# Optimization experiments

Measured on AMD Instinct MI355X. Metric: run time of the kernel, lower is better.

## Reference

```python
import jax, jax.numpy as jnp
import numpy as np

HEADS = 12
DIM_HEAD = 64
SCALE = DIM_HEAD ** -0.5


def _layer_norm(x, w):
    # LayerNorm with learned weight and zero bias (bias is a frozen zeros buffer)
    mu = jnp.mean(x, axis=-1, keepdims=True)
    var = jnp.var(x, axis=-1, keepdims=True)
    return (x - mu) * jax.lax.rsqrt(var + 1e-5) * w


def setup_inputs() -> dict:
    key = jax.random.key(0)
    ks = jax.random.split(key, 6)
    b, n, j, dim = 4, 2048, 2048, 768
    inner = HEADS * DIM_HEAD  # 768
    return {
        "x": jax.random.normal(ks[0], (b, n, dim), dtype=jnp.float32),
        "context": jax.random.normal(ks[1], (b, j, dim), dtype=jnp.float32),
        "mask": jnp.zeros((b, n, j), dtype=jnp.float32),
        "ln_w": jnp.ones((dim,), dtype=jnp.float32),
        "Wq": jax.random.normal(ks[2], (dim, inner), dtype=jnp.float32) * (dim ** -0.5),
        "Wkv": jax.random.normal(ks[3], (dim, 2 * DIM_HEAD), dtype=jnp.float32) * (dim ** -0.5),
        "Wo": jax.random.normal(ks[4], (inner, dim), dtype=jnp.float32) * (inner ** -0.5),
    }


def reference(x, context, mask, ln_w, Wq, Wkv, Wo):
    b, n, dim = x.shape
    xn = _layer_norm(x, ln_w)
    # context_norm is Identity (norm_context=False)
    q = xn @ Wq  # [b, n, h*d]
    q = q.reshape(b, n, HEADS, DIM_HEAD).transpose(0, 2, 1, 3) * SCALE  # [b,h,n,d]
    kv = context @ Wkv  # [b, j, 2d]
    k, v = jnp.split(kv, 2, axis=-1)  # each [b, j, d] (multi-query: shared K/V)
    sim = jnp.einsum('bhid,bjd->bhij', q, k) + mask[:, None, :, :]
    # softmax with max-subtraction (jax.nn.softmax is max-stabilized, same math)
    attn = jax.nn.softmax(sim, axis=-1)
    out = jnp.einsum('bhij,bjd->bhid', attn, v)
    out = out.transpose(0, 2, 1, 3).reshape(b, n, HEADS * DIM_HEAD)
    out = out @ Wo
    # ff is None (parallel_ff=False)
    return out
```

## Files before the change

kernel.cpp:

```cpp
#include <hip/hip_runtime.h>


typedef unsigned short u16;
typedef unsigned int u32;
typedef __attribute__((ext_vector_type(8))) short short8;
typedef __attribute__((ext_vector_type(4))) short short4v;
typedef __attribute__((ext_vector_type(4))) float f32x4;
typedef __attribute__((ext_vector_type(2))) u32 u32x2;

#define L2E 1.44269504088896340736f

__device__ __forceinline__ u16 f2bf(float f) {
  u32 u = __float_as_uint(f);
  u += 0x7FFFu + ((u >> 16) & 1u);
  return (u16)(u >> 16);
}
__device__ __forceinline__ f32x4 mfma16(short8 a, short8 b, f32x4 c) {
  return __builtin_amdgcn_mfma_f32_16x16x32_bf16(a, b, c, 0, 0, 0);
}
__device__ __forceinline__ f32x4 mfma16k16(short4v a, short4v b, f32x4 c) {
  return __builtin_amdgcn_mfma_f32_16x16x16bf16_1k(a, b, c, 0, 0, 0);
}
__device__ __forceinline__ void gl2lds16(const u16* g, u16* s) {
  __builtin_amdgcn_global_load_lds(
      (const __attribute__((address_space(1))) u32*)g,
      (__attribute__((address_space(3))) u32*)s, 16, 0, 0);
}
__device__ __forceinline__ u32 pk2bf(float a, float b) {
  return ((__float_as_uint(a) + 0x8000u) >> 16) |
         ((__float_as_uint(b) + 0x8000u) & 0xffff0000u);
}

__device__ __forceinline__ void wt_tile(const float* in, u16* out, int K,
                                        int N, int tn, int tk,
                                        u16 (*tile)[72]) {
  const int t = threadIdx.x;
  const int tn0 = tn * 64, tk0 = tk * 64;
#pragma unroll
  for (int p = 0; p < 16; p++) {
    int e = p * 256 + t;
    int k = e >> 6, n = e & 63;
    tile[n][k] = f2bf(in[(size_t)(tk0 + k) * N + tn0 + n]);
  }
  __syncthreads();
#pragma unroll
  for (int p = 0; p < 16; p++) {
    int e = p * 256 + t;
    int n = e >> 6, k = e & 63;
    out[(size_t)(tn0 + n) * K + tk0 + k] = tile[n][k];
  }
}

__global__ __launch_bounds__(256)
void prep_kernel(const float* __restrict__ Wq, const float* __restrict__ Wkv,
                 const float* __restrict__ Wo, const float* __restrict__ ctx,
                 const float* __restrict__ x, const float* __restrict__ lnw,
                 u16* __restrict__ WqT, u16* __restrict__ WkvT,
                 u16* __restrict__ WoT, u16* __restrict__ ctxb,
                 u16* __restrict__ xn) {
  __shared__ u16 tile[64][72];
  __shared__ float red[8];
  __shared__ float sh_mu, sh_rs;
  const int bid = blockIdx.x, t = threadIdx.x;
  if (bid < 288) {
    const float* in = bid < 144 ? Wq : Wo;
    u16* out = bid < 144 ? WqT : WoT;
    int id = bid < 144 ? bid : bid - 144;
    wt_tile(in, out, 768, 768, id % 12, id / 12, tile);
  } else if (bid < 312) {
    int id = bid - 288;
    wt_tile(Wkv, WkvT, 768, 128, id % 2, id / 2, tile);
  } else if (bid < 6456) {
    int i = (bid - 312) * 256 + t;
    float4 v = ((const float4*)ctx)[i];
    ushort4 o;
    o.x = f2bf(v.x); o.y = f2bf(v.y); o.z = f2bf(v.z); o.w = f2bf(v.w);
    ((ushort4*)ctxb)[i] = o;
  } else {
    const int row = bid - 6456;
    const float* xr = x + (size_t)row * 768;
    float v0 = xr[t], v1 = xr[t + 256], v2 = xr[t + 512];
    float s = v0 + v1 + v2;
    float q = v0 * v0 + v1 * v1 + v2 * v2;
#pragma unroll
    for (int off = 32; off; off >>= 1) {
      s += __shfl_down(s, off);
      q += __shfl_down(q, off);
    }
    int wv = t >> 6;
    if ((t & 63) == 0) { red[wv * 2] = s; red[wv * 2 + 1] = q; }
    __syncthreads();
    if (t == 0) {
      float S = red[0] + red[2] + red[4] + red[6];
      float Q = red[1] + red[3] + red[5] + red[7];
      float mu = S * (1.0f / 768.0f);
      float var = Q * (1.0f / 768.0f) - mu * mu;
      sh_mu = mu;
      sh_rs = rsqrtf(var + 1e-5f);
    }
    __syncthreads();
    float mu = sh_mu, rs = sh_rs;
    u16* o = xn + (size_t)row * 768;
    o[t]       = f2bf((v0 - mu) * rs * lnw[t]);
    o[t + 256] = f2bf((v1 - mu) * rs * lnw[t + 256]);
    o[t + 512] = f2bf((v2 - mu) * rs * lnw[t + 512]);
  }
}

template <int BM, int BN>
__device__ __forceinline__ void gemm_stage(const u16* A, const u16* Bt, int K,
                                           int m0, int n0, int k0, u16* As,
                                           u16* Bs, int w, int l) {
  constexpr int CHA = BM * 8;
  constexpr int ISS = (BM + BN) * 8 / 256;
#pragma unroll
  for (int i = 0; i < ISS; i++) {
    const int c0 = (i * 4 + w) * 64;
    const int c = c0 + l;
    if (c0 < CHA) {
      int row = c >> 3, cc = c & 7, gc = cc ^ (row & 7);
      gl2lds16(A + (size_t)(m0 + row) * K + k0 + gc * 8, As + c0 * 8);
    } else {
      int cb = c - CHA;
      int row = cb >> 3, cc = cb & 7, gc = cc ^ (row & 7);
      gl2lds16(Bt + (size_t)(n0 + row) * K + k0 + gc * 8, Bs + (c0 - CHA) * 8);
    }
  }
}

template <int BM, int BN>
__device__ __forceinline__ void gemm_core(u16* As0, u16* As1, u16* Bs0,
                                          u16* Bs1, const u16* A,
                                          const u16* Bt, void* C, int N, int K,
                                          float scale, int out_bf16, int bx,
                                          int by) {
  constexpr int MT = BM / 32, NT = BN / 32;
  const int t = threadIdx.x;
  const int w = t >> 6, l = t & 63, lg = l >> 4, lc = l & 15;
  const int wm = w & 1, wn = w >> 1;
  const int n0 = bx * BN, m0 = by * BM;
  u16* Asb[2] = {As0, As1};
  u16* Bsb[2] = {Bs0, Bs1};

  f32x4 acc[MT][NT];
#pragma unroll
  for (int mt = 0; mt < MT; mt++)
#pragma unroll
    for (int nt = 0; nt < NT; nt++) acc[mt][nt] = (f32x4){0.f, 0.f, 0.f, 0.f};

  gemm_stage<BM, BN>(A, Bt, K, m0, n0, 0, As0, Bs0, w, l);
  int p = 0;
  for (int k0 = 0; k0 < K; k0 += 64, p ^= 1) {
    __syncthreads();
    if (k0 + 64 < K)
      gemm_stage<BM, BN>(A, Bt, K, m0, n0, k0 + 64, Asb[p ^ 1], Bsb[p ^ 1], w, l);
    const u16* As = Asb[p];
    const u16* Bs = Bsb[p];
#pragma unroll
    for (int ks = 0; ks < 2; ks++) {
      short8 af[MT], bfr[NT];
#pragma unroll
      for (int mt = 0; mt < MT; mt++) {
        int m = wm * (BM / 2) + mt * 16 + lc;
        af[mt] = *(const short8*)&As[m * 64 + (((ks * 4 + lg) ^ (m & 7)) * 8)];
      }
#pragma unroll
      for (int nt = 0; nt < NT; nt++) {
        int n = wn * (BN / 2) + nt * 16 + lc;
        bfr[nt] = *(const short8*)&Bs[n * 64 + (((ks * 4 + lg) ^ (n & 7)) * 8)];
      }
#pragma unroll
      for (int mt = 0; mt < MT; mt++)
#pragma unroll
        for (int nt = 0; nt < NT; nt++)
          acc[mt][nt] = mfma16(af[mt], bfr[nt], acc[mt][nt]);
    }
  }

#pragma unroll
  for (int mt = 0; mt < MT; mt++)
#pragma unroll
    for (int nt = 0; nt < NT; nt++)
#pragma unroll
      for (int r = 0; r < 4; r++) {
        int row = m0 + wm * (BM / 2) + mt * 16 + lg * 4 + r;
        int col = n0 + wn * (BN / 2) + nt * 16 + lc;
        float v = acc[mt][nt][r] * scale;
        if (out_bf16)
          ((u16*)C)[(size_t)row * N + col] = f2bf(v);
        else
          ((float*)C)[(size_t)row * N + col] = v;
      }
}

__global__ __launch_bounds__(256)
void gemm_qkv_kernel(const u16* __restrict__ xn, const u16* __restrict__ WqT,
                     u16* __restrict__ qb, const u16* __restrict__ ctxb,
                     const u16* __restrict__ WkvT, u16* __restrict__ kvb) {
  __shared__ __align__(16) u16 As[2][128 * 64];
  __shared__ __align__(16) u16 Bs[2][64 * 64];
  if (blockIdx.x < 12)
    gemm_core<128, 64>(As[0], As[1], Bs[0], Bs[1], xn, WqT, qb, 768, 768,
                       0.125f * L2E, 1, blockIdx.x, blockIdx.y);
  else
    gemm_core<128, 64>(As[0], As[1], Bs[0], Bs[1], ctxb, WkvT, kvb, 128, 768,
                       1.0f, 1, blockIdx.x - 12, blockIdx.y);
}

__global__ __launch_bounds__(256)
void gemm_o_kernel(const u16* __restrict__ aob, const u16* __restrict__ WoT,
                   float* __restrict__ out) {
  __shared__ __align__(16) u16 As[2][128 * 64];
  __shared__ __align__(16) u16 Bs[2][64 * 64];
  gemm_core<128, 64>(As[0], As[1], Bs[0], Bs[1], aob, WoT, out, 768, 768, 1.0f,
                     0, blockIdx.x, blockIdx.y);
}

__global__ void tv_kernel(const u16* __restrict__ kv, u16* __restrict__ vT) {
  __shared__ u16 tile[64][72];
  const int t = threadIdx.x;
  const int bb = blockIdx.y, j0 = blockIdx.x << 6;
#pragma unroll
  for (int p = 0; p < 16; p++) {
    int e = p * 256 + t;
    int j = e >> 6, d = e & 63;
    tile[j][d] = kv[(size_t)(bb * 2048 + j0 + j) * 128 + 64 + d];
  }
  __syncthreads();
#pragma unroll
  for (int p = 0; p < 16; p++) {
    int e = p * 256 + t;
    int d = e >> 6, j = e & 63;
    vT[(size_t)(bb * 64 + d) * 2048 + j0 + j] = tile[j][d];
  }
}

__device__ __forceinline__ void attn_stage(const u16* kvb, const u16* vtb,
                                           u16* Kq, u16* Vq, int j0, int w,
                                           int l) {
#pragma unroll
  for (int i = 0; i < 2; i++) {
    int c = i * 64 + l;
    int row = c >> 3, cc = c & 7, gc = cc ^ (row & 7);
    gl2lds16(kvb + (size_t)(j0 + w * 16 + row) * 128 + gc * 8,
             Kq + i * 64 * 8);
  }
#pragma unroll
  for (int i = 0; i < 2; i++) {
    int c = i * 64 + l;
    int d = c >> 1, hf = c & 1;
    gl2lds16(vtb + (size_t)d * 2048 + j0 + w * 16 + hf * 8, Vq + i * 64 * 8);
  }
}

__global__ __launch_bounds__(256, 3)
void attn_kernel(const u16* __restrict__ q, const u16* __restrict__ kv,
                 const u16* __restrict__ vT, const float* __restrict__ mask,
                 u16* __restrict__ ao) {
  __shared__ __align__(16) u16 lds[2][4][2048];

  const int t = threadIdx.x;
  const int i0 = blockIdx.x << 4;
  const int bb = blockIdx.y;
  const int hg = blockIdx.z;
  const int w = t >> 6, l = t & 63, lg = l >> 4, lc = l & 15;

  short8 qf[4][2];
#pragma unroll
  for (int hh = 0; hh < 4; hh++) {
    const int h = hg * 4 + hh;
    const u16* qp = q + (size_t)(bb * 2048 + i0 + lc) * 768 + h * 64 + lg * 8;
    qf[hh][0] = *(const short8*)qp;
    qf[hh][1] = *(const short8*)(qp + 32);
  }

  f32x4 o[4][4];
  float lsum[4] = {0.f, 0.f, 0.f, 0.f};
#pragma unroll
  for (int hh = 0; hh < 4; hh++)
#pragma unroll
    for (int nt = 0; nt < 4; nt++) o[hh][nt] = (f32x4){0.f, 0.f, 0.f, 0.f};

  const u16* kvb = kv + (size_t)bb * 2048 * 128;
  const u16* vtb = vT + (size_t)bb * 64 * 2048;
  const float* mrow =
      mask + (size_t)(bb * 2048 + i0 + lc) * 2048 + w * 16 + lg * 4;

  attn_stage(kvb, vtb, &lds[0][w][0], &lds[0][w][1024], 0, w, l);
  float4 mk = *(const float4*)mrow;

  for (int jj = 0; jj < 32; jj++) {
    const int p = jj & 1;
    __syncthreads();
    float4 mk_n = mk;
    if (jj + 1 < 32) {
      attn_stage(kvb, vtb, &lds[p ^ 1][w][0], &lds[p ^ 1][w][1024],
                 (jj + 1) * 64, w, l);
      mk_n = *(const float4*)(mrow + (jj + 1) * 64);
    }
    const u16* Kq = &lds[p][w][0];
    const u16* Vq = &lds[p][w][1024];
    short8 kf0 = *(const short8*)&Kq[lc * 64 + ((lg ^ (lc & 7)) * 8)];
    short8 kf1 = *(const short8*)&Kq[lc * 64 + (((4 + lg) ^ (lc & 7)) * 8)];
    short4v vfr[4];
#pragma unroll
    for (int nt = 0; nt < 4; nt++)
      vfr[nt] = *(const short4v*)&Vq[(nt * 16 + lc) * 16 + lg * 4];

#pragma unroll
    for (int hh = 0; hh < 4; hh++) {
      f32x4 s = mfma16(kf0, qf[hh][0], (f32x4){0.f, 0.f, 0.f, 0.f});
      s = mfma16(kf1, qf[hh][1], s);
      float p0 = __builtin_amdgcn_exp2f(__builtin_fmaf(mk.x, L2E, s[0]));
      float p1 = __builtin_amdgcn_exp2f(__builtin_fmaf(mk.y, L2E, s[1]));
      float p2 = __builtin_amdgcn_exp2f(__builtin_fmaf(mk.z, L2E, s[2]));
      float p3 = __builtin_amdgcn_exp2f(__builtin_fmaf(mk.w, L2E, s[3]));
      lsum[hh] += (p0 + p1) + (p2 + p3);
      u32x2 pp = {pk2bf(p0, p1), pk2bf(p2, p3)};
      short4v pk = __builtin_bit_cast(short4v, pp);
#pragma unroll
      for (int nt = 0; nt < 4; nt++)
        o[hh][nt] = mfma16k16(pk, vfr[nt], o[hh][nt]);
    }
    mk = mk_n;
  }

  float* f = (float*)&lds[0][0][0];
  const int ei = t >> 4, eg = t & 15;
#pragma unroll
  for (int hh = 0; hh < 4; hh++) {
    float lt = lsum[hh];
    lt += __shfl_xor(lt, 16);
    lt += __shfl_xor(lt, 32);
    __syncthreads();
    if (lg == 0) f[4096 + w * 16 + lc] = lt;
#pragma unroll
    for (int nt = 0; nt < 4; nt++)
#pragma unroll
      for (int r = 0; r < 4; r++)
        f[w * 1024 + (lg * 4 + r) * 64 + nt * 16 + lc] = o[hh][nt][r];
    __syncthreads();
    f32x4 sum = *(const f32x4*)&f[ei * 64 + eg * 4];
#pragma unroll
    for (int ww = 1; ww < 4; ww++) {
      f32x4 v2 = *(const f32x4*)&f[ww * 1024 + ei * 64 + eg * 4];
      sum[0] += v2[0]; sum[1] += v2[1]; sum[2] += v2[2]; sum[3] += v2[3];
    }
    float ltot = f[4096 + ei] + f[4096 + 16 + ei] + f[4096 + 32 + ei] +
                 f[4096 + 48 + ei];
    float inv = 1.0f / ltot;
    ushort4 ov;
    ov.x = f2bf(sum[0] * inv);
    ov.y = f2bf(sum[1] * inv);
    ov.z = f2bf(sum[2] * inv);
    ov.w = f2bf(sum[3] * inv);
    const int h = hg * 4 + hh;
    *(ushort4*)&ao[(size_t)(bb * 2048 + i0 + ei) * 768 + h * 64 + eg * 4] = ov;
  }
}

extern "C" void kernel_launch(void* const* d_in, const int* in_sizes, int n_in,
                              void* d_out, int out_size, void* d_ws,
                              size_t ws_size, hipStream_t stream) {
  const float* x    = (const float*)d_in[0];
  const float* ctx  = (const float*)d_in[1];
  const float* mask = (const float*)d_in[2];
  const float* lnw  = (const float*)d_in[3];
  const float* Wq   = (const float*)d_in[4];
  const float* Wkv  = (const float*)d_in[5];
  const float* Wo   = (const float*)d_in[6];

  char* ws = (char*)d_ws;
  u16* WqT  = (u16*)(ws + 0);
  u16* WkvT = (u16*)(ws + 1179648);
  u16* WoT  = (u16*)(ws + 1376256);
  u16* xn   = (u16*)(ws + 2555904);
  u16* ctxb = (u16*)(ws + 15138816);
  u16* qb   = (u16*)(ws + 27721728);
  u16* kvb  = (u16*)(ws + 40304640);
  u16* vTb  = (u16*)(ws + 42401792);
  u16* aob  = (u16*)(ws + 43450368);

  hipLaunchKernelGGL(prep_kernel, dim3(14648), dim3(256), 0, stream,
                     Wq, Wkv, Wo, ctx, x, lnw, WqT, WkvT, WoT, ctxb, xn);
  hipLaunchKernelGGL(gemm_qkv_kernel, dim3(14, 64), dim3(256), 0, stream,
                     xn, WqT, qb, ctxb, WkvT, kvb);
  hipLaunchKernelGGL(tv_kernel, dim3(32, 4), dim3(256), 0, stream, kvb, vTb);
  hipLaunchKernelGGL(attn_kernel, dim3(128, 4, 3), dim3(256), 0, stream,
                     qb, kvb, vTb, mask, aob);
  hipLaunchKernelGGL(gemm_o_kernel, dim3(12, 64), dim3(256), 0, stream,
                     aob, WoT, (float*)d_out);
}
```

Baseline: 291.4 us.

## Prepack K/V into MFMA fragment layout and load directly to registers

Replaces the V-transpose kernel with a pack kernel that writes K and V in per-lane MFMA fragment order. The attention kernel then drops the LDS staging and per-iteration barriers, loading fragments straight from global memory into registers with a one-step register prefetch. It also swaps the manual bf16 packing for the hardware v_cvt_pk_bf16_f32 instruction. The cost is exposed global-load latency, with only one iteration of prefetch and no shared staging, and the packed buffers reuse the ctxb region of the workspace.

```diff
diff --git a/kernel.cpp b/kernel.cpp
--- a/kernel.cpp
+++ b/kernel.cpp
@@ -26,9 +26,12 @@
       (const __attribute__((address_space(1))) u32*)g,
       (__attribute__((address_space(3))) u32*)s, 16, 0, 0);
 }
-__device__ __forceinline__ u32 pk2bf(float a, float b) {
-  return ((__float_as_uint(a) + 0x8000u) >> 16) |
-         ((__float_as_uint(b) + 0x8000u) & 0xffff0000u);
+__device__ __forceinline__ short4v cvt4bf(float a, float b, float c, float d) {
+  u32 lo, hi;
+  asm("v_cvt_pk_bf16_f32 %0, %1, %2" : "=v"(lo) : "v"(a), "v"(b));
+  asm("v_cvt_pk_bf16_f32 %0, %1, %2" : "=v"(hi) : "v"(c), "v"(d));
+  u32x2 pp = {lo, hi};
+  return __builtin_bit_cast(short4v, pp);
 }
 
 __device__ __forceinline__ void wt_tile(const float* in, u16* out, int K,
@@ -216,48 +219,39 @@
                      0, blockIdx.x, blockIdx.y);
 }
 
-__global__ void tv_kernel(const u16* __restrict__ kv, u16* __restrict__ vT) {
-  __shared__ u16 tile[64][72];
-  const int t = threadIdx.x;
-  const int bb = blockIdx.y, j0 = blockIdx.x << 6;
-#pragma unroll
-  for (int p = 0; p < 16; p++) {
-    int e = p * 256 + t;
-    int j = e >> 6, d = e & 63;
-    tile[j][d] = kv[(size_t)(bb * 2048 + j0 + j) * 128 + 64 + d];
-  }
-  __syncthreads();
-#pragma unroll
-  for (int p = 0; p < 16; p++) {
-    int e = p * 256 + t;
-    int d = e >> 6, j = e & 63;
-    vT[(size_t)(bb * 64 + d) * 2048 + j0 + j] = tile[j][d];
-  }
-}
-
-__device__ __forceinline__ void attn_stage(const u16* kvb, const u16* vtb,
-                                           u16* Kq, u16* Vq, int j0, int w,
-                                           int l) {
-#pragma unroll
-  for (int i = 0; i < 2; i++) {
-    int c = i * 64 + l;
-    int row = c >> 3, cc = c & 7, gc = cc ^ (row & 7);
-    gl2lds16(kvb + (size_t)(j0 + w * 16 + row) * 128 + gc * 8,
-             Kq + i * 64 * 8);
-  }
-#pragma unroll
-  for (int i = 0; i < 2; i++) {
-    int c = i * 64 + l;
-    int d = c >> 1, hf = c & 1;
-    gl2lds16(vtb + (size_t)d * 2048 + j0 + w * 16 + hf * 8, Vq + i * 64 * 8);
+__global__ void pack_kernel(const u16* __restrict__ kv, u16* __restrict__ kF,
+                            u16* __restrict__ vF) {
+  const int t = threadIdx.x, l = t & 63, cw = t >> 6;
+  const int b = blockIdx.y, jb0 = blockIdx.x * 4;
+  const int lc = l & 15, lg = l >> 4;
+#pragma unroll
+  for (int c = cw; c < 8; c += 4) {
+    int jb = jb0 + (c >> 1), half = c & 1;
+    const u16* src =
+        kv + (size_t)(b * 2048 + jb * 16 + lc) * 128 + half * 32 + lg * 8;
+    u16* dst = kF + (((size_t)(b * 128 + jb) * 2 + half) * 64 + l) * 8;
+    *(short8*)dst = *(const short8*)src;
+  }
+#pragma unroll
+  for (int c = cw; c < 8; c += 4) {
+    int jb = jb0 + (c >> 1), ntp = c & 1;
+    u16 tmp[8];
+#pragma unroll
+    for (int e = 0; e < 8; e++) {
+      int d = ntp * 32 + (e >> 2) * 16 + lc;
+      int j = jb * 16 + lg * 4 + (e & 3);
+      tmp[e] = kv[(size_t)(b * 2048 + j) * 128 + 64 + d];
+    }
+    u16* dst = vF + (((size_t)(b * 128 + jb) * 2 + ntp) * 64 + l) * 8;
+    *(short8*)dst = *(const short8*)tmp;
   }
 }
 
 __global__ __launch_bounds__(256, 3)
-void attn_kernel(const u16* __restrict__ q, const u16* __restrict__ kv,
-                 const u16* __restrict__ vT, const float* __restrict__ mask,
+void attn_kernel(const u16* __restrict__ q, const u16* __restrict__ kF,
+                 const u16* __restrict__ vF, const float* __restrict__ mask,
                  u16* __restrict__ ao) {
-  __shared__ __align__(16) u16 lds[2][4][2048];
+  __shared__ float f[4160];
 
   const int t = threadIdx.x;
   const int i0 = blockIdx.x << 4;
@@ -281,51 +275,48 @@
 #pragma unroll
     for (int nt = 0; nt < 4; nt++) o[hh][nt] = (f32x4){0.f, 0.f, 0.f, 0.f};
 
-  const u16* kvb = kv + (size_t)bb * 2048 * 128;
-  const u16* vtb = vT + (size_t)bb * 64 * 2048;
+  const u16* kb = kF + ((size_t)(bb * 128 + w) * 2) * 512 + l * 8;
+  const u16* vb = vF + ((size_t)(bb * 128 + w) * 2) * 512 + l * 8;
   const float* mrow =
       mask + (size_t)(bb * 2048 + i0 + lc) * 2048 + w * 16 + lg * 4;
 
-  attn_stage(kvb, vtb, &lds[0][w][0], &lds[0][w][1024], 0, w, l);
+  short8 kc0 = *(const short8*)(kb);
+  short8 kc1 = *(const short8*)(kb + 512);
+  short8 vc0 = *(const short8*)(vb);
+  short8 vc1 = *(const short8*)(vb + 512);
   float4 mk = *(const float4*)mrow;
 
   for (int jj = 0; jj < 32; jj++) {
-    const int p = jj & 1;
-    __syncthreads();
-    float4 mk_n = mk;
-    if (jj + 1 < 32) {
-      attn_stage(kvb, vtb, &lds[p ^ 1][w][0], &lds[p ^ 1][w][1024],
-                 (jj + 1) * 64, w, l);
-      mk_n = *(const float4*)(mrow + (jj + 1) * 64);
-    }
-    const u16* Kq = &lds[p][w][0];
-    const u16* Vq = &lds[p][w][1024];
-    short8 kf0 = *(const short8*)&Kq[lc * 64 + ((lg ^ (lc & 7)) * 8)];
-    short8 kf1 = *(const short8*)&Kq[lc * 64 + (((4 + lg) ^ (lc & 7)) * 8)];
+    const int jn = jj < 31 ? jj + 1 : 31;
+    short8 kn0 = *(const short8*)(kb + (size_t)jn * 4096);
+    short8 kn1 = *(const short8*)(kb + (size_t)jn * 4096 + 512);
+    short8 vn0 = *(const short8*)(vb + (size_t)jn * 4096);
+    short8 vn1 = *(const short8*)(vb + (size_t)jn * 4096 + 512);
+    float4 mkn = *(const float4*)(mrow + (size_t)jn * 64);
+
     short4v vfr[4];
-#pragma unroll
-    for (int nt = 0; nt < 4; nt++)
-      vfr[nt] = *(const short4v*)&Vq[(nt * 16 + lc) * 16 + lg * 4];
+    vfr[0] = __builtin_shufflevector(vc0, vc0, 0, 1, 2, 3);
+    vfr[1] = __builtin_shufflevector(vc0, vc0, 4, 5, 6, 7);
+    vfr[2] = __builtin_shufflevector(vc1, vc1, 0, 1, 2, 3);
+    vfr[3] = __builtin_shufflevector(vc1, vc1, 4, 5, 6, 7);
 
 #pragma unroll
     for (int hh = 0; hh < 4; hh++) {
-      f32x4 s = mfma16(kf0, qf[hh][0], (f32x4){0.f, 0.f, 0.f, 0.f});
-      s = mfma16(kf1, qf[hh][1], s);
+      f32x4 s = mfma16(kc0, qf[hh][0], (f32x4){0.f, 0.f, 0.f, 0.f});
+      s = mfma16(kc1, qf[hh][1], s);
       float p0 = __builtin_amdgcn_exp2f(__builtin_fmaf(mk.x, L2E, s[0]));
       float p1 = __builtin_amdgcn_exp2f(__builtin_fmaf(mk.y, L2E, s[1]));
       float p2 = __builtin_amdgcn_exp2f(__builtin_fmaf(mk.z, L2E, s[2]));
       float p3 = __builtin_amdgcn_exp2f(__builtin_fmaf(mk.w, L2E, s[3]));
       lsum[hh] += (p0 + p1) + (p2 + p3);
-      u32x2 pp = {pk2bf(p0, p1), pk2bf(p2, p3)};
-      short4v pk = __builtin_bit_cast(short4v, pp);
+      short4v pk = cvt4bf(p0, p1, p2, p3);
 #pragma unroll
       for (int nt = 0; nt < 4; nt++)
         o[hh][nt] = mfma16k16(pk, vfr[nt], o[hh][nt]);
     }
-    mk = mk_n;
-  }
-
-  float* f = (float*)&lds[0][0][0];
+    kc0 = kn0; kc1 = kn1; vc0 = vn0; vc1 = vn1; mk = mkn;
+  }
+
   const int ei = t >> 4, eg = t & 15;
 #pragma unroll
   for (int hh = 0; hh < 4; hh++) {
@@ -376,18 +367,20 @@
   u16* WoT  = (u16*)(ws + 1376256);
   u16* xn   = (u16*)(ws + 2555904);
   u16* ctxb = (u16*)(ws + 15138816);
+  u16* kFb  = (u16*)(ws + 15138816);
+  u16* vFb  = (u16*)(ws + 16187392);
   u16* qb   = (u16*)(ws + 27721728);
   u16* kvb  = (u16*)(ws + 40304640);
-  u16* vTb  = (u16*)(ws + 42401792);
   u16* aob  = (u16*)(ws + 43450368);
 
   hipLaunchKernelGGL(prep_kernel, dim3(14648), dim3(256), 0, stream,
                      Wq, Wkv, Wo, ctx, x, lnw, WqT, WkvT, WoT, ctxb, xn);
   hipLaunchKernelGGL(gemm_qkv_kernel, dim3(14, 64), dim3(256), 0, stream,
                      xn, WqT, qb, ctxb, WkvT, kvb);
-  hipLaunchKernelGGL(tv_kernel, dim3(32, 4), dim3(256), 0, stream, kvb, vTb);
+  hipLaunchKernelGGL(pack_kernel, dim3(32, 4), dim3(256), 0, stream,
+                     kvb, kFb, vFb);
   hipLaunchKernelGGL(attn_kernel, dim3(128, 4, 3), dim3(256), 0, stream,
-                     qb, kvb, vTb, mask, aob);
+                     qb, kFb, vFb, mask, aob);
   hipLaunchKernelGGL(gemm_o_kernel, dim3(12, 64), dim3(256), 0, stream,
                      aob, WoT, (float*)d_out);
 }
```

After: 285.0 us. -2.2%, faster.
